# Optimization experiments

Hardware: AMD Instinct MI355X
Metric: run time of the kernel (lower is better)

Reference implementation:

```python
import jax, jax.numpy as jnp
import numpy as np

N_NODES = 50000
N_EDGES = 800000
D_FEAT = 128


def setup_inputs() -> dict:
    key = jax.random.key(0)
    k1, k2, k3, k4 = jax.random.split(key, 4)
    h = jax.random.normal(k1, (N_NODES, D_FEAT), dtype=jnp.float32)
    # degree-style normalizer, strictly positive
    norm = jax.random.uniform(k2, (N_NODES, 1), dtype=jnp.float32, minval=0.05, maxval=1.0)
    eps = jnp.zeros((1,), dtype=jnp.float32)  # init_eps=0, learn_eps=False
    src = jax.random.randint(k3, (N_EDGES,), 0, N_NODES, dtype=jnp.int32)
    dst = jax.random.randint(k4, (N_EDGES,), 0, N_NODES, dtype=jnp.int32)
    return {"h": h, "norm": norm, "eps": eps, "src": src, "dst": dst}


def reference(h, norm, eps, src, dst):
    # h: [N, D], norm: [N, 1], eps: [1], src/dst: [E]
    hn = h * norm                                   # pre-normalize
    # update_all(copy_u('h','m'), sum('m','neigh')): neigh[v] = sum_{(u,v) in E} hn[u]
    neigh = jax.ops.segment_sum(hn[src], dst, num_segments=N_NODES)  # [N, D]
    out = (1.0 + eps) * hn + neigh                  # eps-combine (broadcast [1] scalar)
    out = out * norm                                # post-normalize
    return out
```

## Files before the change

### kernel.cpp

```cpp
#include <hip/hip_runtime.h>

#define D_FEAT  128
#define CAP      64
#define CELLCAP  20
#define EPB    1024

typedef unsigned int u32;

__device__ __forceinline__ u32 f2bf_pack(float a, float b) {
    u32 ua = __float_as_uint(a);
    u32 ub = __float_as_uint(b);
    ua = (ua + 0x7fffu + ((ua >> 16) & 1u)) >> 16;
    ub = (ub + 0x7fffu + ((ub >> 16) & 1u)) >> 16;
    return ua | (ub << 16);
}

__device__ __forceinline__ float bf_lo(u32 p) { return __uint_as_float(p << 16); }
__device__ __forceinline__ float bf_hi(u32 p) { return __uint_as_float(p & 0xffff0000u); }

__global__ void __launch_bounds__(256)
partition_hn(const int* __restrict__ src, const int* __restrict__ dst,
             int* __restrict__ cnt, u32* __restrict__ binbuf,
             const float* __restrict__ h, const float* __restrict__ norm,
             u32* __restrict__ hn, int n_edges, int n_nodes, int nbins, int nba) {
    __shared__ int cur[512];
    int tid = threadIdx.x;
    int blk = blockIdx.x;
    for (int i = tid; i < nbins; i += 256) cur[i] = 0;
    __syncthreads();
    int base = blk * EPB;
    int m = n_edges - base; if (m > EPB) m = EPB;
    for (int k = tid; k < m; k += 256) {
        int d = dst[base + k];
        int s = src[base + k];
        int bin = d >> 7;
        int r = atomicAdd(&cur[bin], 1);
        if (r < CELLCAP)
            binbuf[((size_t)bin * nba + blk) * CELLCAP + r] =
                (u32)s | ((u32)(d & 127) << 16);
    }
    __syncthreads();
    for (int i = tid; i < nbins; i += 256) {
        int c = cur[i]; if (c > CELLCAP) c = CELLCAP;
        cnt[(size_t)i * nba + blk] = c;
    }
    int gsize = gridDim.x * 256;
    int total4 = n_nodes * (D_FEAT / 4);
    for (int j = blk * 256 + tid; j < total4; j += gsize) {
        int node = j >> 5;
        float nm = norm[node];
        float4 v = reinterpret_cast<const float4*>(h)[j];
        uint2 o;
        o.x = f2bf_pack(v.x * nm, v.y * nm);
        o.y = f2bf_pack(v.z * nm, v.w * nm);
        reinterpret_cast<uint2*>(hn)[j] = o;
    }
}

__global__ void __launch_bounds__(256)
bucket_build(const int* __restrict__ cnt, u32* __restrict__ binbuf,
             int* __restrict__ counts, int n_nodes, int nba) {
    __shared__ int lcnt[128];
    __shared__ u32 lbuf[128 * CAP];
    int tid = threadIdx.x;
    int b = blockIdx.x;
    if (tid < 128) lcnt[tid] = 0;
    __syncthreads();
    size_t binbase = (size_t)b * nba * CELLCAP;
    for (int k = tid; k < nba; k += 256) {
        int c = cnt[(size_t)b * nba + k];
        const u32* cell = binbuf + binbase + (size_t)k * CELLCAP;
        for (int j = 0; j < c; ++j) {
            u32 v = cell[j];
            int local = (int)(v >> 16);
            int r = atomicAdd(&lcnt[local], 1);
            if (r < CAP) lbuf[(local << 6) + r] = v & 0xffffu;
        }
    }
    __syncthreads();
    u32* brow = binbuf + binbase;
    for (int slot = tid; slot < 128 * CAP; slot += 256) {
        int local = slot >> 6;
        int r = slot & (CAP - 1);
        int node = (b << 7) + local;
        int c = lcnt[local]; if (c > CAP) c = CAP;
        if (node < n_nodes && r < c) brow[((size_t)local << 6) + r] = lbuf[slot];
    }
    if (tid < 128) {
        int node = (b << 7) + tid;
        if (node < n_nodes) {
            int c = lcnt[tid]; if (c > CAP) c = CAP;
            counts[node] = c;
        }
    }
}

__global__ void gather_v4(const float* __restrict__ h,
                          const float* __restrict__ norm,
                          const float* __restrict__ eps,
                          const int* __restrict__ counts,
                          const u32* __restrict__ store, size_t binstride,
                          const u32* __restrict__ hn,
                          float* __restrict__ out, int n_nodes) {
    int t = blockIdx.x * 256 + threadIdx.x;
    int node = t >> 5;
    int lane = t & 31;
    if (node >= n_nodes) return;
    int cnt = counts[node];
    if (cnt > CAP) cnt = CAP;
    const u32* row = store + (size_t)(node >> 7) * binstride
                           + ((size_t)(node & 127) << 6);
    float a0 = 0.0f, a1 = 0.0f, a2 = 0.0f, a3 = 0.0f;
    int i = 0;
    for (; i + 8 <= cnt; i += 8) {
        u32 s0 = row[i + 0], s1 = row[i + 1], s2 = row[i + 2], s3 = row[i + 3];
        u32 s4 = row[i + 4], s5 = row[i + 5], s6 = row[i + 6], s7 = row[i + 7];
        uint2 p0 = reinterpret_cast<const uint2*>(hn + (size_t)s0 * 64)[lane];
        uint2 p1 = reinterpret_cast<const uint2*>(hn + (size_t)s1 * 64)[lane];
        uint2 p2 = reinterpret_cast<const uint2*>(hn + (size_t)s2 * 64)[lane];
        uint2 p3 = reinterpret_cast<const uint2*>(hn + (size_t)s3 * 64)[lane];
        uint2 p4 = reinterpret_cast<const uint2*>(hn + (size_t)s4 * 64)[lane];
        uint2 p5 = reinterpret_cast<const uint2*>(hn + (size_t)s5 * 64)[lane];
        uint2 p6 = reinterpret_cast<const uint2*>(hn + (size_t)s6 * 64)[lane];
        uint2 p7 = reinterpret_cast<const uint2*>(hn + (size_t)s7 * 64)[lane];
        a0 += bf_lo(p0.x) + bf_lo(p1.x) + bf_lo(p2.x) + bf_lo(p3.x)
            + bf_lo(p4.x) + bf_lo(p5.x) + bf_lo(p6.x) + bf_lo(p7.x);
        a1 += bf_hi(p0.x) + bf_hi(p1.x) + bf_hi(p2.x) + bf_hi(p3.x)
            + bf_hi(p4.x) + bf_hi(p5.x) + bf_hi(p6.x) + bf_hi(p7.x);
        a2 += bf_lo(p0.y) + bf_lo(p1.y) + bf_lo(p2.y) + bf_lo(p3.y)
            + bf_lo(p4.y) + bf_lo(p5.y) + bf_lo(p6.y) + bf_lo(p7.y);
        a3 += bf_hi(p0.y) + bf_hi(p1.y) + bf_hi(p2.y) + bf_hi(p3.y)
            + bf_hi(p4.y) + bf_hi(p5.y) + bf_hi(p6.y) + bf_hi(p7.y);
    }
    for (; i + 4 <= cnt; i += 4) {
        u32 s0 = row[i + 0], s1 = row[i + 1], s2 = row[i + 2], s3 = row[i + 3];
        uint2 p0 = reinterpret_cast<const uint2*>(hn + (size_t)s0 * 64)[lane];
        uint2 p1 = reinterpret_cast<const uint2*>(hn + (size_t)s1 * 64)[lane];
        uint2 p2 = reinterpret_cast<const uint2*>(hn + (size_t)s2 * 64)[lane];
        uint2 p3 = reinterpret_cast<const uint2*>(hn + (size_t)s3 * 64)[lane];
        a0 += bf_lo(p0.x) + bf_lo(p1.x) + bf_lo(p2.x) + bf_lo(p3.x);
        a1 += bf_hi(p0.x) + bf_hi(p1.x) + bf_hi(p2.x) + bf_hi(p3.x);
        a2 += bf_lo(p0.y) + bf_lo(p1.y) + bf_lo(p2.y) + bf_lo(p3.y);
        a3 += bf_hi(p0.y) + bf_hi(p1.y) + bf_hi(p2.y) + bf_hi(p3.y);
    }
    for (; i < cnt; ++i) {
        uint2 p = reinterpret_cast<const uint2*>(hn + (size_t)row[i] * 64)[lane];
        a0 += bf_lo(p.x); a1 += bf_hi(p.x); a2 += bf_lo(p.y); a3 += bf_hi(p.y);
    }
    float nd = norm[node];
    float e1 = 1.0f + eps[0];
    float4 hv = reinterpret_cast<const float4*>(h + (size_t)node * D_FEAT)[lane];
    float4 o;
    o.x = (e1 * hv.x * nd + a0) * nd;
    o.y = (e1 * hv.y * nd + a1) * nd;
    o.z = (e1 * hv.z * nd + a2) * nd;
    o.w = (e1 * hv.w * nd + a3) * nd;
    reinterpret_cast<float4*>(out + (size_t)node * D_FEAT)[lane] = o;
}

__global__ void zero_counts(int* __restrict__ counts, int n) {
    int i = blockIdx.x * 256 + threadIdx.x;
    if (i < n) counts[i] = 0;
}

__global__ void bucket_hn(const int* __restrict__ src, const int* __restrict__ dst,
                          int* __restrict__ counts, u32* __restrict__ bucket,
                          const float* __restrict__ h, const float* __restrict__ norm,
                          u32* __restrict__ hn, int n_edges, int n_nodes) {
    int gsize = gridDim.x * 256;
    int t = blockIdx.x * 256 + threadIdx.x;
    bool have = (t < n_edges);
    int d = 0, p = 0, s = 0;
    if (have) {
        d = dst[t]; s = src[t];
        p = atomicAdd(&counts[d], 1);
    }
    int total4 = n_nodes * (D_FEAT / 4);
    for (int j = t; j < total4; j += gsize) {
        int node = j >> 5;
        float nm = norm[node];
        float4 v = reinterpret_cast<const float4*>(h)[j];
        uint2 o;
        o.x = f2bf_pack(v.x * nm, v.y * nm);
        o.y = f2bf_pack(v.z * nm, v.w * nm);
        reinterpret_cast<uint2*>(hn)[j] = o;
    }
    if (have && p < CAP) bucket[(size_t)d * CAP + p] = (u32)s;
}

__global__ void gin_init(const float* __restrict__ h, const float* __restrict__ norm,
                         const float* __restrict__ eps, float* __restrict__ out,
                         int n_nodes) {
    int i = blockIdx.x * blockDim.x + threadIdx.x;
    int total = n_nodes * (D_FEAT / 4);
    if (i >= total) return;
    int node = i / (D_FEAT / 4);
    float nm = norm[node];
    float scale = (1.0f + eps[0]) * nm * nm;
    const float4* h4 = reinterpret_cast<const float4*>(h);
    float4* o4 = reinterpret_cast<float4*>(out);
    float4 v = h4[i];
    v.x *= scale; v.y *= scale; v.z *= scale; v.w *= scale;
    o4[i] = v;
}

__global__ void gin_edge(const float* __restrict__ h, const float* __restrict__ norm,
                         const int* __restrict__ src, const int* __restrict__ dst,
                         float* __restrict__ out, int n_edges) {
    long long t = (long long)blockIdx.x * blockDim.x + threadIdx.x;
    int e = (int)(t >> 5);
    int lane = (int)(t & 31);
    if (e >= n_edges) return;
    int s = src[e], d = dst[e];
    float coef = norm[s] * norm[d];
    const float4* hs = reinterpret_cast<const float4*>(h + (long long)s * D_FEAT);
    float4 v = hs[lane];
    float* od = out + (long long)d * D_FEAT + lane * 4;
    atomicAdd(od + 0, v.x * coef);
    atomicAdd(od + 1, v.y * coef);
    atomicAdd(od + 2, v.z * coef);
    atomicAdd(od + 3, v.w * coef);
}

extern "C" void kernel_launch(void* const* d_in, const int* in_sizes, int n_in,
                              void* d_out, int out_size, void* d_ws, size_t ws_size,
                              hipStream_t stream) {
    const float* h    = (const float*)d_in[0];
    const float* norm = (const float*)d_in[1];
    const float* eps  = (const float*)d_in[2];
    const int*   src  = (const int*)d_in[3];
    const int*   dst  = (const int*)d_in[4];
    float* out = (float*)d_out;

    int n_nodes = in_sizes[1];
    int n_edges = in_sizes[3];

    int nbins = (n_nodes + 127) >> 7;
    int nba   = (n_edges + EPB - 1) / EPB;
    size_t binstride = (size_t)nba * CELLCAP;

    size_t hn_words = (size_t)n_nodes * (D_FEAT / 2);
    size_t need1 = (hn_words
                    + (size_t)nbins * binstride
                    + (size_t)nbins * nba
                    + (size_t)n_nodes) * 4;
    size_t need2 = (hn_words + (size_t)n_nodes + (size_t)n_nodes * CAP) * 4;

    int gb = (n_nodes + 7) / 8;
    int eb = (n_edges + 255) / 256;
    int pre_threads = n_nodes * (D_FEAT / 4);

    bool tier1_ok = (n_nodes <= 65536) && (nbins <= 512)
                    && (binstride >= 128 * CAP)
                    && (ws_size >= need1);

    if (tier1_ok) {
        u32* hn     = (u32*)d_ws;
        u32* binbuf = hn + hn_words;
        int* cnt    = (int*)(binbuf + (size_t)nbins * binstride);
        int* counts = cnt + (size_t)nbins * nba;

        partition_hn<<<nba, 256, 0, stream>>>(src, dst, cnt, binbuf, h, norm, hn,
                                              n_edges, n_nodes, nbins, nba);
        bucket_build<<<nbins, 256, 0, stream>>>(cnt, binbuf, counts, n_nodes, nba);
        gather_v4<<<gb, 256, 0, stream>>>(h, norm, eps, counts, binbuf, binstride,
                                          hn, out, n_nodes);
    } else if (ws_size >= need2) {
        u32* hn     = (u32*)d_ws;
        int* counts = (int*)(hn + hn_words);
        u32* bucket = (u32*)(counts + n_nodes);

        zero_counts<<<(n_nodes + 255) / 256, 256, 0, stream>>>(counts, n_nodes);
        bucket_hn<<<eb, 256, 0, stream>>>(src, dst, counts, bucket, h, norm, hn,
                                          n_edges, n_nodes);
        gather_v4<<<gb, 256, 0, stream>>>(h, norm, eps, counts, bucket,
                                          (size_t)128 * CAP, hn, out, n_nodes);
    } else {
        gin_init<<<(pre_threads + 255) / 256, 256, 0, stream>>>(h, norm, eps, out, n_nodes);
        long long et = (long long)n_edges * 32;
        gin_edge<<<(int)((et + 255) / 256), 256, 0, stream>>>(h, norm, src, dst, out, n_edges);
    }
}
```

Before: 72.58 us.

## Fuse bucket build and gather into one per-bin kernel using LDS indices

Merges the bucket_build and gather_v4 kernels into a single bin_gather kernel. Each 1024-thread block assembles its 128-node adjacency lists in shared memory as 16-bit local indices and gathers from them directly. This drops one launch and the global write and read-back of the bucketed index lists and counts. In exchange, only nbins (about 391) large blocks do the gather, so occupancy and load balance may suffer, and the u16 source index relies on the node count fitting in 16 bits.

```diff
diff --git a/kernel.cpp b/kernel.cpp
--- a/kernel.cpp
+++ b/kernel.cpp
@@ -6,6 +6,7 @@
 #define EPB    1024
 
 typedef unsigned int u32;
+typedef unsigned short u16;
 
 __device__ __forceinline__ u32 f2bf_pack(float a, float b) {
     u32 ua = __float_as_uint(a);
@@ -57,105 +58,82 @@
     }
 }
 
-__global__ void __launch_bounds__(256)
-bucket_build(const int* __restrict__ cnt, u32* __restrict__ binbuf,
-             int* __restrict__ counts, int n_nodes, int nba) {
+__global__ void __launch_bounds__(1024)
+bin_gather(const int* __restrict__ cnt, const u32* __restrict__ binbuf,
+           const float* __restrict__ h, const float* __restrict__ norm,
+           const float* __restrict__ eps, const u32* __restrict__ hn,
+           float* __restrict__ out, int n_nodes, int nba) {
     __shared__ int lcnt[128];
-    __shared__ u32 lbuf[128 * CAP];
+    __shared__ u16 lbuf[128 * CAP];
     int tid = threadIdx.x;
     int b = blockIdx.x;
     if (tid < 128) lcnt[tid] = 0;
     __syncthreads();
     size_t binbase = (size_t)b * nba * CELLCAP;
-    for (int k = tid; k < nba; k += 256) {
+    for (int k = tid; k < nba; k += 1024) {
         int c = cnt[(size_t)b * nba + k];
         const u32* cell = binbuf + binbase + (size_t)k * CELLCAP;
         for (int j = 0; j < c; ++j) {
             u32 v = cell[j];
             int local = (int)(v >> 16);
             int r = atomicAdd(&lcnt[local], 1);
-            if (r < CAP) lbuf[(local << 6) + r] = v & 0xffffu;
-        }
-    }
-    __syncthreads();
-    u32* brow = binbuf + binbase;
-    for (int slot = tid; slot < 128 * CAP; slot += 256) {
-        int local = slot >> 6;
-        int r = slot & (CAP - 1);
+            if (r < CAP) lbuf[(local << 6) + r] = (u16)(v & 0xffffu);
+        }
+    }
+    __syncthreads();
+    int lane = tid & 31;
+    float e1 = 1.0f + eps[0];
+    for (int local = tid >> 5; local < 128; local += 32) {
         int node = (b << 7) + local;
-        int c = lcnt[local]; if (c > CAP) c = CAP;
-        if (node < n_nodes && r < c) brow[((size_t)local << 6) + r] = lbuf[slot];
-    }
-    if (tid < 128) {
-        int node = (b << 7) + tid;
-        if (node < n_nodes) {
-            int c = lcnt[tid]; if (c > CAP) c = CAP;
-            counts[node] = c;
-        }
-    }
-}
-
-__global__ void gather_v4(const float* __restrict__ h,
-                          const float* __restrict__ norm,
-                          const float* __restrict__ eps,
-                          const int* __restrict__ counts,
-                          const u32* __restrict__ store, size_t binstride,
-                          const u32* __restrict__ hn,
-                          float* __restrict__ out, int n_nodes) {
-    int t = blockIdx.x * 256 + threadIdx.x;
-    int node = t >> 5;
-    int lane = t & 31;
-    if (node >= n_nodes) return;
-    int cnt = counts[node];
-    if (cnt > CAP) cnt = CAP;
-    const u32* row = store + (size_t)(node >> 7) * binstride
-                           + ((size_t)(node & 127) << 6);
-    float a0 = 0.0f, a1 = 0.0f, a2 = 0.0f, a3 = 0.0f;
-    int i = 0;
-    for (; i + 8 <= cnt; i += 8) {
-        u32 s0 = row[i + 0], s1 = row[i + 1], s2 = row[i + 2], s3 = row[i + 3];
-        u32 s4 = row[i + 4], s5 = row[i + 5], s6 = row[i + 6], s7 = row[i + 7];
-        uint2 p0 = reinterpret_cast<const uint2*>(hn + (size_t)s0 * 64)[lane];
-        uint2 p1 = reinterpret_cast<const uint2*>(hn + (size_t)s1 * 64)[lane];
-        uint2 p2 = reinterpret_cast<const uint2*>(hn + (size_t)s2 * 64)[lane];
-        uint2 p3 = reinterpret_cast<const uint2*>(hn + (size_t)s3 * 64)[lane];
-        uint2 p4 = reinterpret_cast<const uint2*>(hn + (size_t)s4 * 64)[lane];
-        uint2 p5 = reinterpret_cast<const uint2*>(hn + (size_t)s5 * 64)[lane];
-        uint2 p6 = reinterpret_cast<const uint2*>(hn + (size_t)s6 * 64)[lane];
-        uint2 p7 = reinterpret_cast<const uint2*>(hn + (size_t)s7 * 64)[lane];
-        a0 += bf_lo(p0.x) + bf_lo(p1.x) + bf_lo(p2.x) + bf_lo(p3.x)
-            + bf_lo(p4.x) + bf_lo(p5.x) + bf_lo(p6.x) + bf_lo(p7.x);
-        a1 += bf_hi(p0.x) + bf_hi(p1.x) + bf_hi(p2.x) + bf_hi(p3.x)
-            + bf_hi(p4.x) + bf_hi(p5.x) + bf_hi(p6.x) + bf_hi(p7.x);
-        a2 += bf_lo(p0.y) + bf_lo(p1.y) + bf_lo(p2.y) + bf_lo(p3.y)
-            + bf_lo(p4.y) + bf_lo(p5.y) + bf_lo(p6.y) + bf_lo(p7.y);
-        a3 += bf_hi(p0.y) + bf_hi(p1.y) + bf_hi(p2.y) + bf_hi(p3.y)
-            + bf_hi(p4.y) + bf_hi(p5.y) + bf_hi(p6.y) + bf_hi(p7.y);
-    }
-    for (; i + 4 <= cnt; i += 4) {
-        u32 s0 = row[i + 0], s1 = row[i + 1], s2 = row[i + 2], s3 = row[i + 3];
-        uint2 p0 = reinterpret_cast<const uint2*>(hn + (size_t)s0 * 64)[lane];
-        uint2 p1 = reinterpret_cast<const uint2*>(hn + (size_t)s1 * 64)[lane];
-        uint2 p2 = reinterpret_cast<const uint2*>(hn + (size_t)s2 * 64)[lane];
-        uint2 p3 = reinterpret_cast<const uint2*>(hn + (size_t)s3 * 64)[lane];
-        a0 += bf_lo(p0.x) + bf_lo(p1.x) + bf_lo(p2.x) + bf_lo(p3.x);
-        a1 += bf_hi(p0.x) + bf_hi(p1.x) + bf_hi(p2.x) + bf_hi(p3.x);
-        a2 += bf_lo(p0.y) + bf_lo(p1.y) + bf_lo(p2.y) + bf_lo(p3.y);
-        a3 += bf_hi(p0.y) + bf_hi(p1.y) + bf_hi(p2.y) + bf_hi(p3.y);
-    }
-    for (; i < cnt; ++i) {
-        uint2 p = reinterpret_cast<const uint2*>(hn + (size_t)row[i] * 64)[lane];
-        a0 += bf_lo(p.x); a1 += bf_hi(p.x); a2 += bf_lo(p.y); a3 += bf_hi(p.y);
-    }
-    float nd = norm[node];
-    float e1 = 1.0f + eps[0];
-    float4 hv = reinterpret_cast<const float4*>(h + (size_t)node * D_FEAT)[lane];
-    float4 o;
-    o.x = (e1 * hv.x * nd + a0) * nd;
-    o.y = (e1 * hv.y * nd + a1) * nd;
-    o.z = (e1 * hv.z * nd + a2) * nd;
-    o.w = (e1 * hv.w * nd + a3) * nd;
-    reinterpret_cast<float4*>(out + (size_t)node * D_FEAT)[lane] = o;
+        if (node >= n_nodes) continue;
+        int cnt_n = lcnt[local]; if (cnt_n > CAP) cnt_n = CAP;
+        const u16* row = lbuf + (local << 6);
+        float a0 = 0.0f, a1 = 0.0f, a2 = 0.0f, a3 = 0.0f;
+        int i = 0;
+        for (; i + 8 <= cnt_n; i += 8) {
+            int s0 = row[i + 0], s1 = row[i + 1], s2 = row[i + 2], s3 = row[i + 3];
+            int s4 = row[i + 4], s5 = row[i + 5], s6 = row[i + 6], s7 = row[i + 7];
+            uint2 p0 = reinterpret_cast<const uint2*>(hn + (size_t)s0 * 64)[lane];
+            uint2 p1 = reinterpret_cast<const uint2*>(hn + (size_t)s1 * 64)[lane];
+            uint2 p2 = reinterpret_cast<const uint2*>(hn + (size_t)s2 * 64)[lane];
+            uint2 p3 = reinterpret_cast<const uint2*>(hn + (size_t)s3 * 64)[lane];
+            uint2 p4 = reinterpret_cast<const uint2*>(hn + (size_t)s4 * 64)[lane];
+            uint2 p5 = reinterpret_cast<const uint2*>(hn + (size_t)s5 * 64)[lane];
+            uint2 p6 = reinterpret_cast<const uint2*>(hn + (size_t)s6 * 64)[lane];
+            uint2 p7 = reinterpret_cast<const uint2*>(hn + (size_t)s7 * 64)[lane];
+            a0 += bf_lo(p0.x) + bf_lo(p1.x) + bf_lo(p2.x) + bf_lo(p3.x)
+                + bf_lo(p4.x) + bf_lo(p5.x) + bf_lo(p6.x) + bf_lo(p7.x);
+            a1 += bf_hi(p0.x) + bf_hi(p1.x) + bf_hi(p2.x) + bf_hi(p3.x)
+                + bf_hi(p4.x) + bf_hi(p5.x) + bf_hi(p6.x) + bf_hi(p7.x);
+            a2 += bf_lo(p0.y) + bf_lo(p1.y) + bf_lo(p2.y) + bf_lo(p3.y)
+                + bf_lo(p4.y) + bf_lo(p5.y) + bf_lo(p6.y) + bf_lo(p7.y);
+            a3 += bf_hi(p0.y) + bf_hi(p1.y) + bf_hi(p2.y) + bf_hi(p3.y)
+                + bf_hi(p4.y) + bf_hi(p5.y) + bf_hi(p6.y) + bf_hi(p7.y);
+        }
+        for (; i + 4 <= cnt_n; i += 4) {
+            int s0 = row[i + 0], s1 = row[i + 1], s2 = row[i + 2], s3 = row[i + 3];
+            uint2 p0 = reinterpret_cast<const uint2*>(hn + (size_t)s0 * 64)[lane];
+            uint2 p1 = reinterpret_cast<const uint2*>(hn + (size_t)s1 * 64)[lane];
+            uint2 p2 = reinterpret_cast<const uint2*>(hn + (size_t)s2 * 64)[lane];
+            uint2 p3 = reinterpret_cast<const uint2*>(hn + (size_t)s3 * 64)[lane];
+            a0 += bf_lo(p0.x) + bf_lo(p1.x) + bf_lo(p2.x) + bf_lo(p3.x);
+            a1 += bf_hi(p0.x) + bf_hi(p1.x) + bf_hi(p2.x) + bf_hi(p3.x);
+            a2 += bf_lo(p0.y) + bf_lo(p1.y) + bf_lo(p2.y) + bf_lo(p3.y);
+            a3 += bf_hi(p0.y) + bf_hi(p1.y) + bf_hi(p2.y) + bf_hi(p3.y);
+        }
+        for (; i < cnt_n; ++i) {
+            uint2 p = reinterpret_cast<const uint2*>(hn + (size_t)row[i] * 64)[lane];
+            a0 += bf_lo(p.x); a1 += bf_hi(p.x); a2 += bf_lo(p.y); a3 += bf_hi(p.y);
+        }
+        float nd = norm[node];
+        float4 hv = reinterpret_cast<const float4*>(h + (size_t)node * D_FEAT)[lane];
+        float4 o;
+        o.x = (e1 * hv.x * nd + a0) * nd;
+        o.y = (e1 * hv.y * nd + a1) * nd;
+        o.z = (e1 * hv.z * nd + a2) * nd;
+        o.w = (e1 * hv.w * nd + a3) * nd;
+        reinterpret_cast<float4*>(out + (size_t)node * D_FEAT)[lane] = o;
+    }
 }
 
 __global__ void zero_counts(int* __restrict__ counts, int n) {
@@ -186,6 +164,48 @@
         reinterpret_cast<uint2*>(hn)[j] = o;
     }
     if (have && p < CAP) bucket[(size_t)d * CAP + p] = (u32)s;
+}
+
+__global__ void gather_v4(const float* __restrict__ h,
+                          const float* __restrict__ norm,
+                          const float* __restrict__ eps,
+                          const int* __restrict__ counts,
+                          const u32* __restrict__ bucket,
+                          const u32* __restrict__ hn,
+                          float* __restrict__ out, int n_nodes) {
+    int t = blockIdx.x * 256 + threadIdx.x;
+    int node = t >> 5;
+    int lane = t & 31;
+    if (node >= n_nodes) return;
+    int cnt = counts[node];
+    if (cnt > CAP) cnt = CAP;
+    const u32* row = bucket + (size_t)node * CAP;
+    float a0 = 0.0f, a1 = 0.0f, a2 = 0.0f, a3 = 0.0f;
+    int i = 0;
+    for (; i + 4 <= cnt; i += 4) {
+        u32 s0 = row[i + 0], s1 = row[i + 1], s2 = row[i + 2], s3 = row[i + 3];
+        uint2 p0 = reinterpret_cast<const uint2*>(hn + (size_t)s0 * 64)[lane];
+        uint2 p1 = reinterpret_cast<const uint2*>(hn + (size_t)s1 * 64)[lane];
+        uint2 p2 = reinterpret_cast<const uint2*>(hn + (size_t)s2 * 64)[lane];
+        uint2 p3 = reinterpret_cast<const uint2*>(hn + (size_t)s3 * 64)[lane];
+        a0 += bf_lo(p0.x) + bf_lo(p1.x) + bf_lo(p2.x) + bf_lo(p3.x);
+        a1 += bf_hi(p0.x) + bf_hi(p1.x) + bf_hi(p2.x) + bf_hi(p3.x);
+        a2 += bf_lo(p0.y) + bf_lo(p1.y) + bf_lo(p2.y) + bf_lo(p3.y);
+        a3 += bf_hi(p0.y) + bf_hi(p1.y) + bf_hi(p2.y) + bf_hi(p3.y);
+    }
+    for (; i < cnt; ++i) {
+        uint2 p = reinterpret_cast<const uint2*>(hn + (size_t)row[i] * 64)[lane];
+        a0 += bf_lo(p.x); a1 += bf_hi(p.x); a2 += bf_lo(p.y); a3 += bf_hi(p.y);
+    }
+    float nd = norm[node];
+    float e1 = 1.0f + eps[0];
+    float4 hv = reinterpret_cast<const float4*>(h + (size_t)node * D_FEAT)[lane];
+    float4 o;
+    o.x = (e1 * hv.x * nd + a0) * nd;
+    o.y = (e1 * hv.y * nd + a1) * nd;
+    o.z = (e1 * hv.z * nd + a2) * nd;
+    o.w = (e1 * hv.w * nd + a3) * nd;
+    reinterpret_cast<float4*>(out + (size_t)node * D_FEAT)[lane] = o;
 }
 
 __global__ void gin_init(const float* __restrict__ h, const float* __restrict__ norm,
@@ -237,34 +257,28 @@
 
     int nbins = (n_nodes + 127) >> 7;
     int nba   = (n_edges + EPB - 1) / EPB;
-    size_t binstride = (size_t)nba * CELLCAP;
 
     size_t hn_words = (size_t)n_nodes * (D_FEAT / 2);
     size_t need1 = (hn_words
-                    + (size_t)nbins * binstride
-                    + (size_t)nbins * nba
-                    + (size_t)n_nodes) * 4;
+                    + (size_t)nbins * nba * CELLCAP
+                    + (size_t)nbins * nba) * 4;
     size_t need2 = (hn_words + (size_t)n_nodes + (size_t)n_nodes * CAP) * 4;
 
+    int eb = (n_edges + 255) / 256;
     int gb = (n_nodes + 7) / 8;
-    int eb = (n_edges + 255) / 256;
     int pre_threads = n_nodes * (D_FEAT / 4);
 
-    bool tier1_ok = (n_nodes <= 65536) && (nbins <= 512)
-                    && (binstride >= 128 * CAP)
-                    && (ws_size >= need1);
+    bool tier1_ok = (n_nodes <= 65536) && (nbins <= 512) && (ws_size >= need1);
 
     if (tier1_ok) {
         u32* hn     = (u32*)d_ws;
         u32* binbuf = hn + hn_words;
-        int* cnt    = (int*)(binbuf + (size_t)nbins * binstride);
-        int* counts = cnt + (size_t)nbins * nba;
+        int* cnt    = (int*)(binbuf + (size_t)nbins * nba * CELLCAP);
 
         partition_hn<<<nba, 256, 0, stream>>>(src, dst, cnt, binbuf, h, norm, hn,
                                               n_edges, n_nodes, nbins, nba);
-        bucket_build<<<nbins, 256, 0, stream>>>(cnt, binbuf, counts, n_nodes, nba);
-        gather_v4<<<gb, 256, 0, stream>>>(h, norm, eps, counts, binbuf, binstride,
-                                          hn, out, n_nodes);
+        bin_gather<<<nbins, 1024, 0, stream>>>(cnt, binbuf, h, norm, eps, hn,
+                                               out, n_nodes, nba);
     } else if (ws_size >= need2) {
         u32* hn     = (u32*)d_ws;
         int* counts = (int*)(hn + hn_words);
@@ -273,8 +287,8 @@
         zero_counts<<<(n_nodes + 255) / 256, 256, 0, stream>>>(counts, n_nodes);
         bucket_hn<<<eb, 256, 0, stream>>>(src, dst, counts, bucket, h, norm, hn,
                                           n_edges, n_nodes);
-        gather_v4<<<gb, 256, 0, stream>>>(h, norm, eps, counts, bucket,
-                                          (size_t)128 * CAP, hn, out, n_nodes);
+        gather_v4<<<gb, 256, 0, stream>>>(h, norm, eps, counts, bucket, hn,
+                                          out, n_nodes);
     } else {
         gin_init<<<(pre_threads + 255) / 256, 256, 0, stream>>>(h, norm, eps, out, n_nodes);
         long long et = (long long)n_edges * 32;
```

After: 61.39 us, median of 2. -15.4%, faster.
